# Performance work log

Measured on AMD Instinct MI355X. Metric: run time of the kernel, lower is better.

## Reference

```python
import jax, jax.numpy as jnp
import numpy as np

NUM_HEADS = 8
WINDOW = 3
LOCAL_LEN = WINDOW * WINDOW
SR_RATIO = 8


def _normalize(v, eps=1e-12):
    n = jnp.linalg.norm(v, axis=-1, keepdims=True)
    return v / jnp.maximum(n, eps)


def _layernorm(v, g, b, eps=1e-5):
    m = v.mean(-1, keepdims=True)
    var = ((v - m) ** 2).mean(-1, keepdims=True)
    return (v - m) / jnp.sqrt(var + eps) * g + b


def _unfold3(x, H, W):
    # x: [B, C, H, W] -> [B, C, 9, H*W]  (kernel 3, pad 1, stride 1; torch nn.Unfold layout)
    B, C = x.shape[0], x.shape[1]
    xp = jnp.pad(x, ((0, 0), (0, 0), (1, 1), (1, 1)))
    patches = jnp.stack([xp[:, :, di:di + H, dj:dj + W]
                         for di in range(WINDOW) for dj in range(WINDOW)], axis=2)
    return patches.reshape(B, C, LOCAL_LEN, H * W)


def _forward(x, relative_coords_table, seq_length_scale, q_w, q_b, kv_w, kv_b,
             temperature, query_embedding, sr_w, sr_b, norm_g, norm_b,
             cpb_fc1_w, cpb_fc1_b, cpb_fc2_w, cpb_fc2_b,
             rel_bias_local, learnable_tokens, learnable_bias,
             proj_w, proj_b, relative_pos_index, padding_mask, H, W):
    B, N, C = x.shape
    hd = C // NUM_HEADS
    pool_H, pool_W = H // SR_RATIO, W // SR_RATIO
    pool_len = pool_H * pool_W

    # ---- queries ----
    q = (x @ q_w.T + q_b).reshape(B, N, NUM_HEADS, hd).transpose(0, 2, 1, 3)  # [B,h,N,d]
    q_norm = _normalize(q)
    q_scaled = (q_norm + query_embedding) * jax.nn.softplus(temperature) * seq_length_scale

    # ---- local k/v via unfold ----
    kv = x @ kv_w.T + kv_b  # [B,N,2C]
    k_loc = _normalize(kv[..., :C].reshape(B, N, NUM_HEADS, hd)).reshape(B, N, C)
    kv_img = jnp.concatenate([k_loc, kv[..., C:]], -1).transpose(0, 2, 1).reshape(B, 2 * C, H, W)
    kv_unf = _unfold3(kv_img, H, W).reshape(B, 2 * NUM_HEADS, hd, LOCAL_LEN, N)
    kv_unf = kv_unf.transpose(0, 1, 4, 2, 3)  # [B,2h,N,d,9]
    k_local, v_local = kv_unf[:, :NUM_HEADS], kv_unf[:, NUM_HEADS:]

    attn_local = jnp.einsum('bhnd,bhndl->bhnl', q_scaled, k_local) + rel_bias_local[:, None, :]
    attn_local = jnp.where(padding_mask, -jnp.inf, attn_local)

    # ---- pooled global k/v ----
    x_img = x.transpose(0, 2, 1).reshape(B, C, H, W)
    x_sr = jax.nn.gelu(jnp.einsum('oc,bchw->bohw', sr_w, x_img) + sr_b[None, :, None, None],
                       approximate=False)
    x_pool = x_sr.reshape(B, C, pool_H, SR_RATIO, pool_W, SR_RATIO).mean((3, 5))
    x_pool = x_pool.reshape(B, C, pool_len).transpose(0, 2, 1)
    x_pool = _layernorm(x_pool, norm_g, norm_b)
    kv_p = (x_pool @ kv_w.T + kv_b).reshape(B, pool_len, 2 * NUM_HEADS, hd).transpose(0, 2, 1, 3)
    k_pool, v_pool = kv_p[:, :NUM_HEADS], kv_p[:, NUM_HEADS:]

    # ---- continuous relative position bias (extrapolation path) ----
    cpb = jax.nn.relu(relative_coords_table @ cpb_fc1_w.T + cpb_fc1_b) @ cpb_fc2_w.T + cpb_fc2_b  # [T,h]
    pool_bias = cpb[relative_pos_index].reshape(N, pool_len, NUM_HEADS).transpose(2, 0, 1)  # [h,N,P]

    attn_pool = jnp.einsum('bhnd,bhpd->bhnp', q_scaled, _normalize(k_pool)) + pool_bias

    attn = jax.nn.softmax(jnp.concatenate([attn_local, attn_pool], -1), axis=-1)
    a_loc, a_pool = attn[..., :LOCAL_LEN], attn[..., LOCAL_LEN:]

    lt = jnp.einsum('bhnd,hdl->bhnl', q_norm, learnable_tokens) + learnable_bias + a_loc
    x_local = jnp.einsum('bhnl,bhndl->bhnd', lt, v_local)
    x_p = jnp.einsum('bhnp,bhpd->bhnd', a_pool, v_pool)
    out = (x_local + x_p).transpose(0, 2, 1, 3).reshape(B, N, C)
    return out @ proj_w.T + proj_b


def setup_inputs() -> dict:
    key = jax.random.key(0)
    B, H, W, C = 4, 64, 64, 256
    N = H * W
    hd = C // NUM_HEADS
    pool_H, pool_W = H // SR_RATIO, W // SR_RATIO
    pool_len = pool_H * pool_W

    # padding mask + per-query valid window length (get_seqlen_and_mask)
    ii, jj = np.meshgrid(np.arange(H), np.arange(W), indexing='ij')
    cols = []
    for di in range(WINDOW):
        for dj in range(WINDOW):
            ni, nj = ii + di - 1, jj + dj - 1
            cols.append(((ni < 0) | (ni >= H) | (nj < 0) | (nj >= W)).reshape(-1))
    padding_mask = np.stack(cols, -1)  # [N, 9], True = outside image
    local_len = (~padding_mask).sum(-1, keepdims=True).astype(np.float32)
    seq_length_scale = np.log(local_len + pool_len)  # [N, 1]

    # get_relative_position_cpb((H,W), (pool_H,pool_W))
    axis_q = np.arange(H, dtype=np.float64)
    axis_k = axis_q.reshape(pool_H, SR_RATIO).mean(-1)
    kh, kw = np.meshgrid(axis_k, axis_k, indexing='ij')
    qh, qw = np.meshgrid(axis_q, axis_q, indexing='ij')
    rel_h = (qh.ravel()[:, None] - kh.ravel()[None, :]) / (H - 1) * 8
    rel_w = (qw.ravel()[:, None] - kw.ravel()[None, :]) / (W - 1) * 8
    rel = np.stack([rel_h, rel_w], -1).reshape(-1, 2)
    table, idx = np.unique(rel, axis=0, return_inverse=True)
    table = np.sign(table) * np.log2(np.abs(table) + 1.0) / np.log2(8.0)

    ks = jax.random.split(key, 12)

    def nrm(k, shape, std=0.02):
        return jax.random.normal(k, shape, jnp.float32) * std

    return {
        'x': jax.random.normal(ks[0], (B, N, C), jnp.float32),
        'relative_coords_table': jnp.asarray(table, jnp.float32),
        'seq_length_scale': jnp.asarray(seq_length_scale, jnp.float32),
        'q_w': nrm(ks[1], (C, C)), 'q_b': jnp.zeros((C,), jnp.float32),
        'kv_w': nrm(ks[2], (2 * C, C)), 'kv_b': jnp.zeros((2 * C,), jnp.float32),
        'temperature': jnp.full((NUM_HEADS, 1, 1), float(np.log(np.expm1(1.0 / 0.24))), jnp.float32),
        'query_embedding': nrm(ks[3], (NUM_HEADS, 1, hd)),
        'sr_w': nrm(ks[4], (C, C)), 'sr_b': jnp.zeros((C,), jnp.float32),
        'norm_g': jnp.ones((C,), jnp.float32), 'norm_b': jnp.zeros((C,), jnp.float32),
        'cpb_fc1_w': nrm(ks[5], (512, 2), 0.1), 'cpb_fc1_b': jnp.zeros((512,), jnp.float32),
        'cpb_fc2_w': nrm(ks[6], (NUM_HEADS, 512)), 'cpb_fc2_b': jnp.zeros((NUM_HEADS,), jnp.float32),
        'rel_bias_local': nrm(ks[7], (NUM_HEADS, LOCAL_LEN), 0.0004),
        'learnable_tokens': nrm(ks[8], (NUM_HEADS, hd, LOCAL_LEN)),
        'learnable_bias': jnp.zeros((NUM_HEADS, 1, LOCAL_LEN), jnp.float32),
        'proj_w': nrm(ks[9], (C, C)), 'proj_b': jnp.zeros((C,), jnp.float32),
        'relative_pos_index': jnp.asarray(idx, jnp.int32),
        'padding_mask': jnp.asarray(padding_mask),
        'H': H, 'W': W,
    }


def reference(x, relative_coords_table, seq_length_scale, q_w, q_b, kv_w, kv_b,
              temperature, query_embedding, sr_w, sr_b, norm_g, norm_b,
              cpb_fc1_w, cpb_fc1_b, cpb_fc2_w, cpb_fc2_b,
              rel_bias_local, learnable_tokens, learnable_bias,
              proj_w, proj_b, relative_pos_index, padding_mask, H, W):
    return _forward(x, relative_coords_table, seq_length_scale, q_w, q_b, kv_w, kv_b,
                    temperature, query_embedding, sr_w, sr_b, norm_g, norm_b,
                    cpb_fc1_w, cpb_fc1_b, cpb_fc2_w, cpb_fc2_b,
                    rel_bias_local, learnable_tokens, learnable_bias,
                    proj_w, proj_b, relative_pos_index, padding_mask, H, W)
```

## Files before the change

### kernel.cpp

```cpp
#include <hip/hip_runtime.h>
#include <math.h>


typedef unsigned short ushort_t;
typedef __attribute__((ext_vector_type(8))) _Float16 half8;
typedef __attribute__((ext_vector_type(2))) _Float16 half2_t;
typedef __attribute__((ext_vector_type(4))) float f32x4;
typedef __attribute__((ext_vector_type(4))) int int4_t;

static __device__ __forceinline__ ushort_t f2h(float f) {
    _Float16 h = (_Float16)f;
    return *(ushort_t*)&h;
}

static __device__ __forceinline__ float fdot2f(half2_t a, half2_t b, float c) {
#if __has_builtin(__builtin_amdgcn_fdot2)
    return __builtin_amdgcn_fdot2(a, b, c, false);
#else
    return (float)a[0] * (float)b[0] + (float)a[1] * (float)b[1] + c;
#endif
}

template <int CTRL>
static __device__ __forceinline__ float dpp_addf(float x) {
    int v = __builtin_amdgcn_update_dpp(
        0, __builtin_bit_cast(int, x), CTRL, 0xF, 0xF, true);
    return x + __builtin_bit_cast(float, v);
}
template <int CTRL>
static __device__ __forceinline__ float dpp_maxf(float x) {
    int v = __builtin_amdgcn_update_dpp(
        0, __builtin_bit_cast(int, x), CTRL, 0xF, 0xF, true);
    return fmaxf(x, __builtin_bit_cast(float, v));
}
static __device__ __forceinline__ float quad_sumf(float x) {
    return dpp_addf<0x4E>(dpp_addf<0xB1>(x));
}
static __device__ __forceinline__ float sum16f(float x) {
    return dpp_addf<0x128>(dpp_addf<0x124>(quad_sumf(x)));
}
static __device__ __forceinline__ float max16f(float x) {
    return dpp_maxf<0x128>(dpp_maxf<0x124>(dpp_maxf<0x4E>(dpp_maxf<0xB1>(x))));
}

#define GLOAD16(g, l)                                                        \
    __builtin_amdgcn_global_load_lds(                                        \
        (const __attribute__((address_space(1))) unsigned int*)(g),          \
        (__attribute__((address_space(3))) unsigned int*)(l), 16, 0, 0)

template <int TM, int TN, bool AHM>
__global__ __launch_bounds__(256) void mfma_hgemm(
    const ushort_t* __restrict__ Ag, const ushort_t* __restrict__ Bg,
    const float* __restrict__ bias, float* __restrict__ out0,
    ushort_t* __restrict__ qh_out, ushort_t* __restrict__ kvh,
    ushort_t* __restrict__ xsrh, int mode, int Arows)
{
    const int K = 256;
    const int IM = TM / 32;
    const int JN = TN / 32;
    constexpr int LPS = TM / 64 + TN / 64;
    __shared__ ushort_t Ah[2][TM * 32];
    __shared__ ushort_t Bh[2][TN * 32];

    const int t = threadIdx.x;
    const int w = t >> 6;
    const int lane = t & 63;

    const int nwg = gridDim.x * gridDim.y;
    int wg = blockIdx.y * gridDim.x + blockIdx.x;
    wg = (wg & 7) * (nwg >> 3) + (wg >> 3);
    const int bm = (wg / gridDim.x) * TM;
    const int bn = (wg % gridDim.x) * TN;

    const int wm = (w >> 1) * (TM / 2);
    const int wn = (w & 1) * (TN / 2);

    f32x4 acc[IM][JN];
#pragma unroll
    for (int i = 0; i < IM; ++i)
#pragma unroll
        for (int j = 0; j < JN; ++j) acc[i][j] = f32x4{0.f, 0.f, 0.f, 0.f};

    const int lrow  = t >> 2;
    const int lk8sw = ((t & 3) ^ ((t >> 3) & 3)) * 8;

#define STAGE(bufi, k0s)                                                     \
    do {                                                                     \
        _Pragma("unroll")                                                    \
        for (int r = 0; r < TM / 64; ++r) {                                  \
            const ushort_t* srcA = AHM                                       \
                ? Ag + ((size_t)((k0s) >> 5) * Arows + (bm + r * 64 + lrow)) * 32 + lk8sw \
                : Ag + (size_t)(bm + r * 64 + lrow) * K + (k0s) + lk8sw;     \
            GLOAD16(srcA, &Ah[bufi][(unsigned)(r * 64 + w * 16) * 32]);      \
        }                                                                    \
        _Pragma("unroll")                                                    \
        for (int r = 0; r < TN / 64; ++r)                                    \
            GLOAD16(Bg + (size_t)(bn + r * 64 + lrow) * K + (k0s) + lk8sw,   \
                    &Bh[bufi][(unsigned)(r * 64 + w * 16) * 32]);            \
    } while (0)

    const int fr   = lane & 15;
    const int sws8 = ((lane >> 4) ^ ((fr >> 1) & 3)) * 8;

#define COMPUTE(bufi)                                                        \
    do {                                                                     \
        half8 af[IM], bf[JN];                                                \
        _Pragma("unroll")                                                    \
        for (int i2 = 0; i2 < IM; ++i2)                                      \
            af[i2] = *(const half8*)&Ah[bufi][(unsigned)(wm + i2 * 16 + fr) * 32 + sws8]; \
        _Pragma("unroll")                                                    \
        for (int j2 = 0; j2 < JN; ++j2)                                      \
            bf[j2] = *(const half8*)&Bh[bufi][(unsigned)(wn + j2 * 16 + fr) * 32 + sws8]; \
        __builtin_amdgcn_s_setprio(1);                                       \
        _Pragma("unroll")                                                    \
        for (int i2 = 0; i2 < IM; ++i2)                                      \
            _Pragma("unroll")                                                \
            for (int j2 = 0; j2 < JN; ++j2)                                  \
                acc[i2][j2] = __builtin_amdgcn_mfma_f32_16x16x32_f16(        \
                    af[i2], bf[j2], acc[i2][j2], 0, 0, 0);                   \
        __builtin_amdgcn_s_setprio(0);                                       \
    } while (0)

    STAGE(0, 0);
    STAGE(1, 32);
    int buf = 0;
#pragma unroll
    for (int s = 0; s < K / 32 - 1; ++s) {
        asm volatile("s_waitcnt vmcnt(%0)" :: "n"(LPS) : "memory");
        __builtin_amdgcn_s_barrier();
        asm volatile("" ::: "memory");
        COMPUTE(buf);
        asm volatile("" ::: "memory");
        __builtin_amdgcn_s_barrier();
        asm volatile("" ::: "memory");
        if (s + 2 < K / 32) STAGE(buf, (s + 2) * 32);
        buf ^= 1;
    }
    asm volatile("s_waitcnt vmcnt(0)" ::: "memory");
    __builtin_amdgcn_s_barrier();
    asm volatile("" ::: "memory");
    COMPUTE(buf);
#undef COMPUTE
#undef STAGE

    const int q4 = (lane >> 4) * 4;
#pragma unroll
    for (int i = 0; i < IM; ++i) {
#pragma unroll
        for (int jp = 0; jp < JN / 2; ++jp) {
#pragma unroll
            for (int r = 0; r < 4; ++r) {
                const int row = bm + wm + i * 16 + q4 + r;
                const int col0 = bn + wn + jp * 32 + fr;
                const int col1 = col0 + 16;
                float v0 = acc[i][2 * jp][r] + bias[col0];
                float v1 = acc[i][2 * jp + 1][r] + bias[col1];
                if (mode == 0) {
                    if (col0 < 256) {
                        const size_t base = ((size_t)(col0 >> 5) * Arows + row) * 32;
                        qh_out[base + fr]      = f2h(v0);
                        qh_out[base + fr + 16] = f2h(v1);
                    } else if (col0 < 512) {
                        const float ss = sum16f(v0 * v0 + v1 * v1);
                        const float invn = 1.0f / fmaxf(sqrtf(ss), 1e-12f);
                        const size_t base = ((size_t)((col0 - 256) >> 5) * Arows + row) * 64;
                        kvh[base + fr]      = f2h(v0 * invn);
                        kvh[base + fr + 16] = f2h(v1 * invn);
                    } else if (col0 < 768) {
                        const size_t base = ((size_t)((col0 - 512) >> 5) * Arows + row) * 64 + 32;
                        kvh[base + fr]      = f2h(v0);
                        kvh[base + fr + 16] = f2h(v1);
                    } else {
                        v0 = 0.5f * v0 * (1.0f + erff(v0 * 0.70710678118654752f));
                        v1 = 0.5f * v1 * (1.0f + erff(v1 * 0.70710678118654752f));
                        xsrh[(size_t)row * 256 + (col0 - 768)] = f2h(v0);
                        xsrh[(size_t)row * 256 + (col1 - 768)] = f2h(v1);
                    }
                } else if (mode == 2) {
                    if (col0 < 256) {
                        const float ss = sum16f(v0 * v0 + v1 * v1);
                        const float invn = 1.0f / fmaxf(sqrtf(ss), 1e-12f);
                        const size_t base = ((size_t)(col0 >> 5) * Arows + row) * 64;
                        kvh[base + fr]      = f2h(v0 * invn);
                        kvh[base + fr + 16] = f2h(v1 * invn);
                    } else {
                        const size_t base = ((size_t)((col0 - 256) >> 5) * Arows + row) * 64 + 32;
                        kvh[base + fr]      = f2h(v0);
                        kvh[base + fr + 16] = f2h(v1);
                    }
                } else {
                    out0[(size_t)row * 256 + col0] = v0;
                    out0[(size_t)row * 256 + col1] = v1;
                }
            }
        }
    }
}

__global__ __launch_bounds__(256) void prep_cpb(
    const float4* __restrict__ x, ushort4* __restrict__ xh, int n4, int nprep,
    const float* __restrict__ qw, const float* __restrict__ kvw,
    const float* __restrict__ srw, const float* __restrict__ pw,
    const float* __restrict__ qb, const float* __restrict__ kvb,
    const float* __restrict__ srb,
    const int* __restrict__ rpi, ushort_t* __restrict__ rpi16,
    ushort_t* __restrict__ Wall, ushort_t* __restrict__ Pw,
    float* __restrict__ ball,
    const float* __restrict__ table, const float* __restrict__ w1,
    const float* __restrict__ b1, const float* __restrict__ w2,
    const float* __restrict__ b2, ushort_t* __restrict__ cpbT, int T)
{
    if (blockIdx.x >= nprep) {
        const int wv = threadIdx.x >> 6;
        const int lane = threadIdx.x & 63;
        const int row = (blockIdx.x - nprep) * 4 + wv;
        if (row >= T) return;
        const float t0 = table[(size_t)row * 2];
        const float t1 = table[(size_t)row * 2 + 1];
        const int base = lane * 8;

        const float4* w1p = (const float4*)(w1 + (size_t)base * 2);
        float4 wa = w1p[0], wb = w1p[1], wc = w1p[2], wd = w1p[3];
        float4 ba = *(const float4*)(b1 + base);
        float4 bb = *(const float4*)(b1 + base + 4);
        float h[8];
        h[0] = fmaxf(fmaf(t1, wa.y, fmaf(t0, wa.x, ba.x)), 0.f);
        h[1] = fmaxf(fmaf(t1, wa.w, fmaf(t0, wa.z, ba.y)), 0.f);
        h[2] = fmaxf(fmaf(t1, wb.y, fmaf(t0, wb.x, ba.z)), 0.f);
        h[3] = fmaxf(fmaf(t1, wb.w, fmaf(t0, wb.z, ba.w)), 0.f);
        h[4] = fmaxf(fmaf(t1, wc.y, fmaf(t0, wc.x, bb.x)), 0.f);
        h[5] = fmaxf(fmaf(t1, wc.w, fmaf(t0, wc.z, bb.y)), 0.f);
        h[6] = fmaxf(fmaf(t1, wd.y, fmaf(t0, wd.x, bb.z)), 0.f);
        h[7] = fmaxf(fmaf(t1, wd.w, fmaf(t0, wd.z, bb.w)), 0.f);

#pragma unroll
        for (int hh = 0; hh < 8; ++hh) {
            const float4* w2p = (const float4*)(w2 + (size_t)hh * 512 + base);
            float4 p0 = w2p[0], p1 = w2p[1];
            float s = h[0]*p0.x + h[1]*p0.y + h[2]*p0.z + h[3]*p0.w
                    + h[4]*p1.x + h[5]*p1.y + h[6]*p1.z + h[7]*p1.w;
#pragma unroll
            for (int off = 1; off <= 32; off <<= 1) s += __shfl_xor(s, off);
            if (lane == 0) cpbT[(size_t)hh * T + row] = f2h(s + b2[hh]);
        }
        return;
    }

    int idx = blockIdx.x * 256 + threadIdx.x;
    if (idx < n4) {
        float4 v = x[idx];
        ushort4 h;
        h.x = f2h(v.x); h.y = f2h(v.y); h.z = f2h(v.z); h.w = f2h(v.w);
        xh[idx] = h;
    }
    if (idx < 65536) {
        const int base = idx * 4;
        const int nn = base >> 8, k = base & 255;
        const float* src;
        if (nn < 256)      src = qw + (size_t)nn * 256 + k;
        else if (nn < 768) src = kvw + (size_t)(nn - 256) * 256 + k;
        else               src = srw + (size_t)(nn - 768) * 256 + k;
        const float4 a = *(const float4*)src;
        ushort4 hw;
        hw.x = f2h(a.x); hw.y = f2h(a.y); hw.z = f2h(a.z); hw.w = f2h(a.w);
        *(ushort4*)&Wall[base] = hw;
        const int4 rv = *(const int4*)&rpi[base];
        ushort4 r4;
        r4.x = (ushort_t)rv.x; r4.y = (ushort_t)rv.y;
        r4.z = (ushort_t)rv.z; r4.w = (ushort_t)rv.w;
        *(ushort4*)&rpi16[base] = r4;
    }
    if (idx < 16384) {
        const float4 a = *(const float4*)&pw[(size_t)idx * 4];
        ushort4 hw;
        hw.x = f2h(a.x); hw.y = f2h(a.y); hw.z = f2h(a.z); hw.w = f2h(a.w);
        *(ushort4*)&Pw[(size_t)idx * 4] = hw;
    }
    if (idx < 1024) {
        float bv;
        if (idx < 256)      bv = qb[idx];
        else if (idx < 768) bv = kvb[idx - 256];
        else                bv = srb[idx - 768];
        ball[idx] = bv;
    }
}

__global__ __launch_bounds__(256) void pool_ln(
    const ushort_t* __restrict__ xsr, const float* __restrict__ g,
    const float* __restrict__ be, ushort_t* __restrict__ xpool, int Hh, int Ww)
{
    const int C = 256;
    const int Nn = Hh * Ww;
    int b = blockIdx.x >> 6;
    int pidx = blockIdx.x & 63;
    int ph = pidx >> 3, pw = pidx & 7;
    int tid = threadIdx.x;
    float s = 0.f;
    for (int si = 0; si < 8; ++si) {
        int i = ph * 8 + si;
        const ushort_t* rowp = xsr + ((size_t)b * Nn + (size_t)i * Ww + pw * 8) * C + tid;
#pragma unroll
        for (int sj = 0; sj < 8; ++sj)
            s += (float)(*(const _Float16*)&rowp[(size_t)sj * C]);
    }
    s *= (1.f / 64.f);
    __shared__ float red[256];
    red[tid] = s; __syncthreads();
    for (int st = 128; st; st >>= 1) { if (tid < st) red[tid] += red[tid + st]; __syncthreads(); }
    float mean = red[0] * (1.f / 256.f);
    __syncthreads();
    float dv = s - mean;
    red[tid] = dv * dv; __syncthreads();
    for (int st = 128; st; st >>= 1) { if (tid < st) red[tid] += red[tid + st]; __syncthreads(); }
    float var = red[0] * (1.f / 256.f);
    xpool[(size_t)blockIdx.x * C + tid] = f2h(dv * rsqrtf(var + 1e-5f) * g[tid] + be[tid]);
}

__global__ __launch_bounds__(256) void attn_v12(
    const ushort_t* __restrict__ qh_g,
    const ushort_t* __restrict__ kvh,
    const ushort_t* __restrict__ kvph,
    const ushort_t* __restrict__ rpi16,
    const ushort_t* __restrict__ cpbT,
    const float* __restrict__ sls, const float* __restrict__ temp,
    const float* __restrict__ qe, const float* __restrict__ rbl,
    const float* __restrict__ ltok, const float* __restrict__ lbias,
    ushort_t* __restrict__ attno,
    int Mtot, int T)
{
    const int h = blockIdx.y, b = blockIdx.z;
    const int t = threadIdx.x;
    const int i = blockIdx.x;
    const int w = t >> 6;
    const int lane = t & 63;

    __shared__ ushort_t kvp[64 * 64];
    __shared__ ushort_t pbPs[64][72];
    __shared__ float mzp[64][2];
    __shared__ float lts[9][32];
    __shared__ float rbl_s[9], lb_s[9], qe_s[32];

    {
        const int lt8 = lane >> 3, ls = lane & 7;
#pragma unroll
        for (int it = 0; it < 2; ++it) {
            const int u = it * 4 + w;
            const int tok = u * 8 + lt8;
            GLOAD16(kvph + ((size_t)h * 256 + b * 64) * 64
                         + (size_t)(tok * 8 + (ls ^ (tok & 7))) * 8,
                    &kvp[(size_t)(u * 8) * 64]);
        }
    }
    {
        const ushort_t* rp16 = rpi16 + (size_t)i * 4096;
        const ushort_t* ctab = cpbT + (size_t)h * T;
        for (int u = t; u < 4096; u += 256)
            pbPs[u >> 6][u & 63] = ctab[rp16[u]];
        for (int u = t; u < 288; u += 256) lts[u % 9][u / 9] = ltok[h * 288 + u];
        if (t < 9)  { rbl_s[t] = rbl[h * 9 + t]; lb_s[t] = lbias[h * 9 + t]; }
        if (t >= 64 && t < 96) qe_s[t - 64] = qe[h * 32 + (t - 64)];
    }
    __syncthreads();

    const int qi = lane >> 2;
    const int g4 = lane & 3;
    const int co = g4 * 8;
    const int j = w * 16 + qi;
    const int n = i * 64 + j;
    const size_t gq = (size_t)b * 4096 + n;
    const ushort_t* kvb = kvh + ((size_t)h * Mtot + (size_t)b * 4096) * 64;

    const float tm = temp[h];
    const float sp = (tm > 20.f) ? tm : log1pf(expf(tm));

    float qv[8];
    {
        const half8 q8 = *(const half8*)(qh_g + ((size_t)h * Mtot + gq) * 32 + co);
        float ss = 0.f;
#pragma unroll
        for (int d = 0; d < 8; ++d) { qv[d] = (float)q8[d]; ss += qv[d] * qv[d]; }
        ss = quad_sumf(ss);
        const float invn = 1.0f / fmaxf(sqrtf(ss), 1e-12f);
#pragma unroll
        for (int d = 0; d < 8; ++d) qv[d] *= invn;
    }

    float lt[9];
#pragma unroll
    for (int l = 0; l < 9; ++l) {
        float dl = 0.f;
        const float4* lw = (const float4*)&lts[l][co];
#pragma unroll
        for (int c4 = 0; c4 < 2; ++c4) {
            float4 w4 = lw[c4];
            dl += qv[4*c4+0]*w4.x + qv[4*c4+1]*w4.y + qv[4*c4+2]*w4.z + qv[4*c4+3]*w4.w;
        }
        dl = quad_sumf(dl);
        lt[l] = dl + lb_s[l];
    }

    const float scal = sp * sls[n];
    half2_t qhp[4];
#pragma unroll
    for (int c = 0; c < 4; ++c) {
        float a = (qv[2*c+0] + qe_s[co + 2*c+0]) * scal;
        float bq = (qv[2*c+1] + qe_s[co + 2*c+1]) * scal;
        qhp[c] = half2_t{(_Float16)a, (_Float16)bq};
    }

    float sl[9];
#pragma unroll
    for (int l = 0; l < 9; ++l) {
        const int di = l / 3 - 1, dj = l % 3 - 1;
        const int ii = i + di;
        const int jn = j + dj;
        const bool ok = (ii >= 0) && (ii < 64) && (jn >= 0) && (jn < 64);
        const int ic = max(min(ii, 63), 0);
        const int jc = max(min(jn, 63), 0);
        const half8 k8 = *(const half8*)&kvb[(size_t)(ic * 64 + jc) * 64 + co];
        float dk = 0.f;
        dk = fdot2f(qhp[0], __builtin_shufflevector(k8, k8, 0, 1), dk);
        dk = fdot2f(qhp[1], __builtin_shufflevector(k8, k8, 2, 3), dk);
        dk = fdot2f(qhp[2], __builtin_shufflevector(k8, k8, 4, 5), dk);
        dk = fdot2f(qhp[3], __builtin_shufflevector(k8, k8, 6, 7), dk);
        dk = quad_sumf(dk);
        sl[l] = ok ? (dk + rbl_s[l]) : -INFINITY;
    }
    float m_l = sl[0];
#pragma unroll
    for (int l = 1; l < 9; ++l) m_l = fmaxf(m_l, sl[l]);

    const int fr = lane & 15;
    const int cn = lane >> 4;
    const int q4 = cn * 4;
    half8 af;
    {
        const int sidx = (4 * fr + cn) << 2;
        int4_t ai;
        ai.x = __builtin_amdgcn_ds_bpermute(sidx, __builtin_bit_cast(int, qhp[0]));
        ai.y = __builtin_amdgcn_ds_bpermute(sidx, __builtin_bit_cast(int, qhp[1]));
        ai.z = __builtin_amdgcn_ds_bpermute(sidx, __builtin_bit_cast(int, qhp[2]));
        ai.w = __builtin_amdgcn_ds_bpermute(sidx, __builtin_bit_cast(int, qhp[3]));
        af = __builtin_bit_cast(half8, ai);
    }
    f32x4 acc[4];
#pragma unroll
    for (int ct = 0; ct < 4; ++ct) {
#pragma unroll
        for (int r = 0; r < 4; ++r)
            acc[ct][r] = (float)(*(const _Float16*)&pbPs[w * 16 + q4 + r][ct * 16 + fr]);
    }
#pragma unroll
    for (int ct = 0; ct < 4; ++ct) {
        const int tok = ct * 16 + fr;
        const half8 bf = *(const half8*)&kvp[(size_t)(tok * 8 + (cn ^ (tok & 7))) * 8];
        acc[ct] = __builtin_amdgcn_mfma_f32_16x16x32_f16(af, bf, acc[ct], 0, 0, 0);
    }

#pragma unroll
    for (int r = 0; r < 4; ++r) {
        float mm = fmaxf(fmaxf(acc[0][r], acc[1][r]), fmaxf(acc[2][r], acc[3][r]));
        mm = max16f(mm);
        float z = 0.f;
        float pv[4];
#pragma unroll
        for (int ct = 0; ct < 4; ++ct) {
            pv[ct] = __expf(acc[ct][r] - mm);
            z += pv[ct];
        }
        z = sum16f(z);
#pragma unroll
        for (int ct = 0; ct < 4; ++ct)
            pbPs[w * 16 + q4 + r][ct * 16 + fr] = f2h(pv[ct]);
        if (fr == 0) { mzp[w * 16 + q4 + r][0] = mm; mzp[w * 16 + q4 + r][1] = z; }
    }

    const float m_p = mzp[j][0];
    const float Z_p = mzp[j][1];
    const float m = fmaxf(m_l, m_p);
    const float fp = __expf(m_p - m);
    float Z = Z_p * fp;
    const _Float16 fh = (_Float16)fp;

    half2_t oh[4];
#pragma unroll
    for (int c = 0; c < 4; ++c) oh[c] = half2_t{(_Float16)0.f, (_Float16)0.f};

#pragma unroll
    for (int cch = 0; cch < 8; ++cch) {
        const half8 p8 = *(const half8*)&pbPs[j][cch * 8];
#pragma unroll
        for (int k = 0; k < 8; ++k) {
            const int p = cch * 8 + k;
            const _Float16 ah = p8[k] * fh;
            const half2_t a2 = half2_t{ah, ah};
            const half8 v8 = *(const half8*)
                &kvp[(size_t)(p * 8 + ((4 + g4) ^ (p & 7))) * 8];
            oh[0] = a2 * __builtin_shufflevector(v8, v8, 0, 1) + oh[0];
            oh[1] = a2 * __builtin_shufflevector(v8, v8, 2, 3) + oh[1];
            oh[2] = a2 * __builtin_shufflevector(v8, v8, 4, 5) + oh[2];
            oh[3] = a2 * __builtin_shufflevector(v8, v8, 6, 7) + oh[3];
        }
    }

#pragma unroll
    for (int l = 0; l < 9; ++l) { sl[l] = __expf(sl[l] - m); Z += sl[l]; }

#pragma unroll
    for (int l = 0; l < 9; ++l) {
        const int di = l / 3 - 1, dj = l % 3 - 1;
        const int ii = i + di;
        const int jn = j + dj;
        const bool ok = (ii >= 0) && (ii < 64) && (jn >= 0) && (jn < 64);
        const int ic = max(min(ii, 63), 0);
        const int jc = max(min(jn, 63), 0);
        const float coef = ok ? (sl[l] + lt[l] * Z) : 0.f;
        const half8 v8 = *(const half8*)&kvb[(size_t)(ic * 64 + jc) * 64 + 32 + co];
        const _Float16 ch = (_Float16)coef;
        const half2_t c2 = half2_t{ch, ch};
        oh[0] = c2 * __builtin_shufflevector(v8, v8, 0, 1) + oh[0];
        oh[1] = c2 * __builtin_shufflevector(v8, v8, 2, 3) + oh[1];
        oh[2] = c2 * __builtin_shufflevector(v8, v8, 4, 5) + oh[2];
        oh[3] = c2 * __builtin_shufflevector(v8, v8, 6, 7) + oh[3];
    }

    const float invZ = 1.0f / Z;
    ushort4* outp = (ushort4*)(attno + ((size_t)h * Mtot + gq) * 32 + co);
#pragma unroll
    for (int c4 = 0; c4 < 2; ++c4) {
        ushort4 u;
        u.x = f2h((float)oh[2*c4+0][0] * invZ);
        u.y = f2h((float)oh[2*c4+0][1] * invZ);
        u.z = f2h((float)oh[2*c4+1][0] * invZ);
        u.w = f2h((float)oh[2*c4+1][1] * invZ);
        outp[c4] = u;
    }
}

extern "C" void kernel_launch(void* const* d_in, const int* in_sizes, int n_in,
                              void* d_out, int out_size, void* d_ws, size_t ws_size,
                              hipStream_t stream)
{
    const float* x    = (const float*)d_in[0];
    const float* tbl  = (const float*)d_in[1];
    const float* sls  = (const float*)d_in[2];
    const float* q_w  = (const float*)d_in[3];
    const float* q_b  = (const float*)d_in[4];
    const float* kv_w = (const float*)d_in[5];
    const float* kv_b = (const float*)d_in[6];
    const float* temp = (const float*)d_in[7];
    const float* qe   = (const float*)d_in[8];
    const float* sr_w = (const float*)d_in[9];
    const float* sr_b = (const float*)d_in[10];
    const float* ng   = (const float*)d_in[11];
    const float* nb   = (const float*)d_in[12];
    const float* f1w  = (const float*)d_in[13];
    const float* f1b  = (const float*)d_in[14];
    const float* f2w  = (const float*)d_in[15];
    const float* f2b  = (const float*)d_in[16];
    const float* rbl  = (const float*)d_in[17];
    const float* ltok = (const float*)d_in[18];
    const float* lbias= (const float*)d_in[19];
    const float* pw   = (const float*)d_in[20];
    const float* pb   = (const float*)d_in[21];
    const int*   rpi  = (const int*)d_in[22];

    const int C = 256, Hh = 64, Ww = 64, Nn = Hh * Ww;
    const int B = in_sizes[0] / (Nn * C);
    const int T = in_sizes[1] / 2;
    const int M = B * Nn;

    float* ws = (float*)d_ws;
    size_t o = 0;
    ushort_t* qh    = (ushort_t*)(ws + o); o += (size_t)M * C / 2;
    ushort_t* kvh   = (ushort_t*)(ws + o); o += (size_t)M * C;
    ushort_t* xsrh  = (ushort_t*)(ws + o); o += (size_t)M * C / 2;
    ushort_t* xpoolh= (ushort_t*)(ws + o); o += (size_t)B * 64 * C / 2;
    ushort_t* kvph  = (ushort_t*)(ws + o); o += (size_t)B * 64 * C;
    ushort_t* cpbT  = (ushort_t*)(ws + o); o += (size_t)T * 4 + 4;
    ushort_t* rpi16 = (ushort_t*)(ws + o); o += 131072;
    ushort_t* xh   = (ushort_t*)(ws + o); o += (size_t)M * C / 2;
    ushort_t* Wall = (ushort_t*)(ws + o); o += 1024 * 256 / 2;
    ushort_t* Pwh  = (ushort_t*)(ws + o); o += 256 * 256 / 2;
    float* ball = ws + o; o += 1024;
    ushort_t* attno_hf = xh;

    dim3 blk(256);
    const int n4x = M * C / 4;
    const int nprep = (n4x + 255) / 256;
    const int ncpb  = (T + 3) / 4;

    prep_cpb<<<nprep + ncpb, blk, 0, stream>>>(
        (const float4*)x, (ushort4*)xh, n4x,
        nprep, q_w, kv_w, sr_w, pw, q_b, kv_b, sr_b, rpi, rpi16,
        Wall, Pwh, ball, tbl, f1w, f1b, f2w, f2b, cpbT, T);
    mfma_hgemm<128, 64, false><<<dim3(16, M / 128), blk, 0, stream>>>(
        xh, Wall, ball, nullptr, qh, kvh, xsrh, 0, M);
    pool_ln<<<B * 64, blk, 0, stream>>>(xsrh, ng, nb, xpoolh, Hh, Ww);
    mfma_hgemm<64, 64, false><<<dim3(8, (B * 64) / 64), blk, 0, stream>>>(
        xpoolh, Wall + 256 * 256, ball + 256, nullptr, nullptr, kvph, nullptr, 2, B * 64);
    attn_v12<<<dim3(64, 8, B), blk, 0, stream>>>(
        qh, kvh, kvph, rpi16, cpbT, sls, temp, qe, rbl, ltok, lbias, attno_hf, M, T);
    mfma_hgemm<64, 64, true><<<dim3(4, M / 64), blk, 0, stream>>>(
        attno_hf, Pwh, pb, (float*)d_out, nullptr, nullptr, nullptr, 1, M);
}
```

Baseline: 208.0 us.

## Fuse pooled LayerNorm with pooled K/V projection into one kernel

The pooled-token LayerNorm kernel now also computes the K/V projection for its row directly, using fdot2 over fp16 weights, and applies per-head L2 normalisation to K in place. This removes the separate small MFMA GEMM launch and the intermediate xpool buffer round-trip. In exchange, each thread reads one full weight row with uncoalesced per-thread accesses. The output indexing hardcodes 256 pooled rows, so it assumes B*64 == 256.

```diff
diff --git a/kernel.cpp b/kernel.cpp
--- a/kernel.cpp
+++ b/kernel.cpp
@@ -176,18 +176,6 @@
                         xsrh[(size_t)row * 256 + (col0 - 768)] = f2h(v0);
                         xsrh[(size_t)row * 256 + (col1 - 768)] = f2h(v1);
                     }
-                } else if (mode == 2) {
-                    if (col0 < 256) {
-                        const float ss = sum16f(v0 * v0 + v1 * v1);
-                        const float invn = 1.0f / fmaxf(sqrtf(ss), 1e-12f);
-                        const size_t base = ((size_t)(col0 >> 5) * Arows + row) * 64;
-                        kvh[base + fr]      = f2h(v0 * invn);
-                        kvh[base + fr + 16] = f2h(v1 * invn);
-                    } else {
-                        const size_t base = ((size_t)((col0 - 256) >> 5) * Arows + row) * 64 + 32;
-                        kvh[base + fr]      = f2h(v0);
-                        kvh[base + fr + 16] = f2h(v1);
-                    }
                 } else {
                     out0[(size_t)row * 256 + col0] = v0;
                     out0[(size_t)row * 256 + col1] = v1;
@@ -285,35 +273,80 @@
     }
 }
 
-__global__ __launch_bounds__(256) void pool_ln(
-    const ushort_t* __restrict__ xsr, const float* __restrict__ g,
-    const float* __restrict__ be, ushort_t* __restrict__ xpool, int Hh, int Ww)
+__global__ __launch_bounds__(256) void pool_ln_kvp(
+    const ushort_t* __restrict__ xsr,
+    const float* __restrict__ g, const float* __restrict__ be,
+    const ushort_t* __restrict__ Wkv,
+    const float* __restrict__ kvbias,
+    ushort_t* __restrict__ kvph,
+    int Hh, int Ww)
 {
     const int C = 256;
     const int Nn = Hh * Ww;
-    int b = blockIdx.x >> 6;
-    int pidx = blockIdx.x & 63;
-    int ph = pidx >> 3, pw = pidx & 7;
-    int tid = threadIdx.x;
+    const int b = blockIdx.x >> 6;
+    const int pidx = blockIdx.x & 63;
+    const int ph = pidx >> 3, pw = pidx & 7;
+    const int tid = threadIdx.x;
+    const int row = blockIdx.x;
+
+    __shared__ float red[256];
+    __shared__ ushort_t row_h[256];
+
     float s = 0.f;
     for (int si = 0; si < 8; ++si) {
-        int i = ph * 8 + si;
+        const int i = ph * 8 + si;
         const ushort_t* rowp = xsr + ((size_t)b * Nn + (size_t)i * Ww + pw * 8) * C + tid;
 #pragma unroll
         for (int sj = 0; sj < 8; ++sj)
             s += (float)(*(const _Float16*)&rowp[(size_t)sj * C]);
     }
     s *= (1.f / 64.f);
-    __shared__ float red[256];
+
     red[tid] = s; __syncthreads();
     for (int st = 128; st; st >>= 1) { if (tid < st) red[tid] += red[tid + st]; __syncthreads(); }
-    float mean = red[0] * (1.f / 256.f);
+    const float mean = red[0] * (1.f / 256.f);
     __syncthreads();
-    float dv = s - mean;
+    const float dv = s - mean;
     red[tid] = dv * dv; __syncthreads();
     for (int st = 128; st; st >>= 1) { if (tid < st) red[tid] += red[tid + st]; __syncthreads(); }
-    float var = red[0] * (1.f / 256.f);
-    xpool[(size_t)blockIdx.x * C + tid] = f2h(dv * rsqrtf(var + 1e-5f) * g[tid] + be[tid]);
+    const float var = red[0] * (1.f / 256.f);
+    row_h[tid] = f2h(dv * rsqrtf(var + 1e-5f) * g[tid] + be[tid]);
+    __syncthreads();
+
+    const ushort_t* wk = Wkv + (size_t)tid * C;
+    const ushort_t* wv = Wkv + (size_t)(256 + tid) * C;
+    float a0 = kvbias[tid];
+    float a1 = kvbias[256 + tid];
+#pragma unroll
+    for (int c8 = 0; c8 < 32; ++c8) {
+        const half8 r8 = *(const half8*)&row_h[c8 * 8];
+        const half8 k8 = *(const half8*)&wk[c8 * 8];
+        const half8 v8 = *(const half8*)&wv[c8 * 8];
+#pragma unroll
+        for (int p = 0; p < 4; ++p) {
+            const half2_t r2 = __builtin_shufflevector(r8, r8, 0, 1);
+            (void)r2;
+        }
+        a0 = fdot2f(__builtin_shufflevector(r8, r8, 0, 1), __builtin_shufflevector(k8, k8, 0, 1), a0);
+        a0 = fdot2f(__builtin_shufflevector(r8, r8, 2, 3), __builtin_shufflevector(k8, k8, 2, 3), a0);
+        a0 = fdot2f(__builtin_shufflevector(r8, r8, 4, 5), __builtin_shufflevector(k8, k8, 4, 5), a0);
+        a0 = fdot2f(__builtin_shufflevector(r8, r8, 6, 7), __builtin_shufflevector(k8, k8, 6, 7), a0);
+        a1 = fdot2f(__builtin_shufflevector(r8, r8, 0, 1), __builtin_shufflevector(v8, v8, 0, 1), a1);
+        a1 = fdot2f(__builtin_shufflevector(r8, r8, 2, 3), __builtin_shufflevector(v8, v8, 2, 3), a1);
+        a1 = fdot2f(__builtin_shufflevector(r8, r8, 4, 5), __builtin_shufflevector(v8, v8, 4, 5), a1);
+        a1 = fdot2f(__builtin_shufflevector(r8, r8, 6, 7), __builtin_shufflevector(v8, v8, 6, 7), a1);
+    }
+
+    float ss = a0 * a0;
+    ss = sum16f(ss);
+    ss += __shfl_xor(ss, 16);
+    const float invn = 1.0f / fmaxf(sqrtf(ss), 1e-12f);
+    const float k_out = a0 * invn;
+
+    const int hh = tid >> 5;
+    const int ch = tid & 31;
+    kvph[((size_t)hh * 256 + row) * 64 + ch]      = f2h(k_out);
+    kvph[((size_t)hh * 256 + row) * 64 + 32 + ch] = f2h(a1);
 }
 
 __global__ __launch_bounds__(256) void attn_v12(
@@ -575,7 +608,6 @@
     ushort_t* qh    = (ushort_t*)(ws + o); o += (size_t)M * C / 2;
     ushort_t* kvh   = (ushort_t*)(ws + o); o += (size_t)M * C;
     ushort_t* xsrh  = (ushort_t*)(ws + o); o += (size_t)M * C / 2;
-    ushort_t* xpoolh= (ushort_t*)(ws + o); o += (size_t)B * 64 * C / 2;
     ushort_t* kvph  = (ushort_t*)(ws + o); o += (size_t)B * 64 * C;
     ushort_t* cpbT  = (ushort_t*)(ws + o); o += (size_t)T * 4 + 4;
     ushort_t* rpi16 = (ushort_t*)(ws + o); o += 131072;
@@ -596,9 +628,8 @@
         Wall, Pwh, ball, tbl, f1w, f1b, f2w, f2b, cpbT, T);
     mfma_hgemm<128, 64, false><<<dim3(16, M / 128), blk, 0, stream>>>(
         xh, Wall, ball, nullptr, qh, kvh, xsrh, 0, M);
-    pool_ln<<<B * 64, blk, 0, stream>>>(xsrh, ng, nb, xpoolh, Hh, Ww);
-    mfma_hgemm<64, 64, false><<<dim3(8, (B * 64) / 64), blk, 0, stream>>>(
-        xpoolh, Wall + 256 * 256, ball + 256, nullptr, nullptr, kvph, nullptr, 2, B * 64);
+    pool_ln_kvp<<<B * 64, blk, 0, stream>>>(
+        xsrh, ng, nb, Wall + 256 * 256, ball + 256, kvph, Hh, Ww);
     attn_v12<<<dim3(64, 8, B), blk, 0, stream>>>(
         qh, kvh, kvph, rpi16, cpbT, sls, temp, qe, rbl, ltok, lbias, attno_hf, M, T);
     mfma_hgemm<64, 64, true><<<dim3(4, M / 64), blk, 0, stream>>>(
```

Measured after the change: 208.5 us. About the same (+0.2%).
